# Kernel tuning notes

Measured on AMD Instinct MI355X. Metric: run time of the kernel, lower is better.

The kernel has to match this reference:

```python
import jax, jax.numpy as jnp
import numpy as np

B, T, LATENT, D, N_ENVS = 128, 64, 16, 512, 4
TOPK_RATIO = 0.1
TEMPERATURE = 1.0


def setup_inputs() -> dict:
    key = jax.random.key(0)
    k1, k2, k3, k4 = jax.random.split(key, 4)
    z_s = jax.random.normal(k1, (B, T, LATENT), dtype=jnp.float32)
    env_idx = jax.random.randint(k2, (B,), 0, N_ENVS, dtype=jnp.int64 if jax.config.jax_enable_x64 else jnp.int32)
    A_base = jax.random.normal(k3, (D, D), dtype=jnp.float32) * 0.1
    A_deltas = jax.random.normal(k4, (N_ENVS, D, D), dtype=jnp.float32) * 0.01  # stacked ParameterList
    return {"z_s": z_s, "env_idx": env_idx, "A_base": A_base, "A_deltas": A_deltas}


def reference(z_s, env_idx, A_base, A_deltas):
    b = z_s.shape[0]
    d = A_base.shape[0]
    # Per-env delta add: the torch loop sums delta_e * (env_idx==e) over envs,
    # which (one env per sample) equals a gather of A_deltas at env_idx.
    A_logits = A_base[None, :, :] + A_deltas[env_idx]          # [B, d, d]
    A_soft = jax.nn.sigmoid(A_logits / TEMPERATURE)            # [B, d, d]
    # Batched top-k sparsification (replaces the per-sample python loop).
    k = max(1, int(TOPK_RATIO * d * d))
    flat = A_logits.reshape(b, d * d)                          # [B, d*d]
    topk_vals, topk_idx = jax.lax.top_k(flat, k)               # [B, k]
    rows = jnp.arange(b)[:, None]                              # [B, 1]
    A_flat = jnp.zeros_like(flat).at[rows, topk_idx].set(jax.nn.sigmoid(topk_vals))
    A = A_flat.reshape(b, d, d)
    return A, A_logits, A_soft
```

## Files before the change

kernel.cpp:

```cpp
#include <hip/hip_runtime.h>
#include <stdint.h>

#define D_DIM   512
#define DD      262144
#define DD4     65536
#define B_DIM   128
#define N_ENVS  4
#define K_SEL   26214
#define BDD     33554432u
#define CAP2    65536
#define CAP3    4096

typedef float nfloat4 __attribute__((ext_vector_type(4)));

#define PK_OFF      64
#define CNT_OFF     128
#define HIST_OFF    192
#define HIST_BYTES  (N_ENVS * 256 * 4)
#define ZERO_BYTES  (HIST_OFF + HIST_BYTES - PK_OFF)
#define PAIRS_OFF   8192
#define PAIRS_BYTES ((size_t)N_ENVS * CAP2 * 8)
#define PLANES_OFF  (PAIRS_OFF + PAIRS_BYTES)
#define PLANES_BYTES ((size_t)N_ENVS * 3 * DD * 4)
#define WS_NEED     (PLANES_OFF + PLANES_BYTES)
#define SEL_NEED    (PAIRS_OFF + PAIRS_BYTES)

__device__ __forceinline__ uint32_t fkey(float f) {
    uint32_t u = __float_as_uint(f);
    return (u & 0x80000000u) ? ~u : (u | 0x80000000u);
}
__device__ __forceinline__ float sigmoidf_(float x) {
    return 1.0f / (1.0f + __expf(-x));
}

__global__ __launch_bounds__(256) void hist8_kernel(
    const float* __restrict__ base, const float* __restrict__ deltas,
    uint32_t* __restrict__ hist8)
{
    int e = blockIdx.y;
    const float4* b4 = (const float4*)base;
    const float4* d4 = (const float4*)(deltas + (size_t)e * DD);
    __shared__ uint32_t s_h[256];
    int tid = threadIdx.x;
    s_h[tid] = 0;
    __syncthreads();
    int g0 = blockIdx.x * 256 + tid;
    #pragma unroll
    for (int r = 0; r < 4; ++r) {
        int g = g0 + r * 16384;
        float4 bv = b4[g], dv = d4[g];
        atomicAdd(&s_h[fkey(bv.x + dv.x) >> 24], 1u);
        atomicAdd(&s_h[fkey(bv.y + dv.y) >> 24], 1u);
        atomicAdd(&s_h[fkey(bv.z + dv.z) >> 24], 1u);
        atomicAdd(&s_h[fkey(bv.w + dv.w) >> 24], 1u);
    }
    __syncthreads();
    if (s_h[tid]) atomicAdd(&hist8[e * 256 + tid], s_h[tid]);
}

__global__ __launch_bounds__(256) void gather8_kernel(
    const float* __restrict__ base, const float* __restrict__ deltas,
    const uint32_t* __restrict__ hist8, uint32_t* __restrict__ pk,
    uint32_t* __restrict__ cnt8, uint2* __restrict__ pairs8)
{
    int e = blockIdx.y;
    const float4* b4 = (const float4*)base;
    const float4* d4 = (const float4*)(deltas + (size_t)e * DD);
    uint2* pp = pairs8 + (size_t)e * CAP2;
    __shared__ uint32_t s_h[256];
    __shared__ uint32_t s_scan[256];
    __shared__ uint32_t s_P, s_base;
    int tid = threadIdx.x;

    s_h[tid] = hist8[e * 256 + tid];
    __syncthreads();
    if (tid == 0) {
        uint32_t cum = 0;
        for (int b = 255; b >= 0; --b) {
            uint32_t c = s_h[b];
            if (cum + c >= (uint32_t)K_SEL) {
                s_P = (uint32_t)b;
                if (blockIdx.x == 0) {
                    pk[2 * e + 0] = (uint32_t)b;
                    pk[2 * e + 1] = (uint32_t)K_SEL - cum;
                }
                break;
            }
            cum += c;
        }
    }
    __syncthreads();
    uint32_t P = s_P;

    int g0 = blockIdx.x * 256 + tid;
    uint32_t m = 0;
    #pragma unroll
    for (int r = 0; r < 4; ++r) {
        int g = g0 + r * 16384;
        float4 bv = b4[g], dv = d4[g];
        m += ((fkey(bv.x + dv.x) >> 24) == P);
        m += ((fkey(bv.y + dv.y) >> 24) == P);
        m += ((fkey(bv.z + dv.z) >> 24) == P);
        m += ((fkey(bv.w + dv.w) >> 24) == P);
    }
    s_scan[tid] = m;
    __syncthreads();
    #pragma unroll
    for (int off = 1; off < 256; off <<= 1) {
        uint32_t v = (tid >= off) ? s_scan[tid - off] : 0u;
        __syncthreads();
        s_scan[tid] += v;
        __syncthreads();
    }
    uint32_t excl = s_scan[tid] - m;
    if (tid == 255) s_base = atomicAdd(&cnt8[e], s_scan[255]);
    __syncthreads();
    uint32_t pos = s_base + excl;

    #pragma unroll
    for (int r = 0; r < 4; ++r) {
        int g = g0 + r * 16384;
        float4 bv = b4[g], dv = d4[g];
        float vs[4] = {bv.x + dv.x, bv.y + dv.y, bv.z + dv.z, bv.w + dv.w};
        #pragma unroll
        for (int j = 0; j < 4; ++j) {
            uint32_t key = fkey(vs[j]);
            if ((key >> 24) == P) {
                if (pos < CAP2) pp[pos] = make_uint2(key, (uint32_t)(g * 4 + j));
                ++pos;
            }
        }
    }
}

__global__ __launch_bounds__(1024) void select2_kernel(
    const uint32_t* __restrict__ pk, const uint32_t* __restrict__ cnt8,
    const uint2* __restrict__ pairs8, uint32_t* __restrict__ thrcut)
{
    int e = blockIdx.x;
    const uint2* pp = pairs8 + (size_t)e * CAP2;
    uint32_t M = cnt8[e]; if (M > CAP2) M = CAP2;
    uint32_t krem8 = pk[2 * e + 1];

    __shared__ uint32_t s_h16[256];
    __shared__ uint2    s_pairs[CAP3];
    __shared__ uint32_t s_b16, s_krem16, s_cnt;
    int tid = threadIdx.x;
    if (tid < 256) s_h16[tid] = 0;
    if (tid == 0) s_cnt = 0;
    __syncthreads();

    for (uint32_t j = tid; j < M; j += 1024)
        atomicAdd(&s_h16[(pp[j].x >> 16) & 255u], 1u);
    __syncthreads();
    if (tid == 0) {
        uint32_t cum = 0;
        for (int b = 255; b >= 0; --b) {
            uint32_t c = s_h16[b];
            if (cum + c >= krem8) { s_b16 = (uint32_t)b; s_krem16 = krem8 - cum; break; }
            cum += c;
        }
    }
    __syncthreads();
    uint32_t b16 = s_b16;
    for (uint32_t j = tid; j < M; j += 1024) {
        uint2 p = pp[j];
        if (((p.x >> 16) & 255u) == b16) {
            uint32_t pos = atomicAdd(&s_cnt, 1u);
            if (pos < CAP3) s_pairs[pos] = p;
        }
    }
    __syncthreads();
    uint32_t M2 = s_cnt; if (M2 > CAP3) M2 = CAP3;
    uint32_t target = s_krem16 - 1;
    for (uint32_t j = tid; j < M2; j += 1024) {
        uint2 me = s_pairs[j];
        uint32_t rank = 0;
        for (uint32_t l = 0; l < M2; ++l) {
            uint2 o = s_pairs[l];
            rank += (o.x > me.x) || (o.x == me.x && o.y < me.y);
        }
        if (rank == target) {
            thrcut[2 * e + 0] = me.x;
            thrcut[2 * e + 1] = me.y;
        }
    }
}

__global__ __launch_bounds__(256) void planes_kernel(
    const float* __restrict__ base, const float* __restrict__ deltas,
    const uint32_t* __restrict__ thrcut, float* __restrict__ planes)
{
    int e = blockIdx.y;
    int g = blockIdx.x * 256 + threadIdx.x;
    uint32_t T = thrcut[2 * e], C = thrcut[2 * e + 1];
    uint32_t i0 = (uint32_t)g * 4u;
    float4 bv = ((const float4*)base)[g];
    float4 dv = ((const float4*)(deltas + (size_t)e * DD))[g];
    nfloat4 lg = { bv.x + dv.x, bv.y + dv.y, bv.z + dv.z, bv.w + dv.w };
    nfloat4 sg = { sigmoidf_(lg.x), sigmoidf_(lg.y),
                   sigmoidf_(lg.z), sigmoidf_(lg.w) };
    uint32_t kx = fkey(lg.x), ky = fkey(lg.y), kz = fkey(lg.z), kw = fkey(lg.w);
    nfloat4 av;
    av.x = (kx > T || (kx == T && i0 + 0u <= C)) ? sg.x : 0.0f;
    av.y = (ky > T || (ky == T && i0 + 1u <= C)) ? sg.y : 0.0f;
    av.z = (kz > T || (kz == T && i0 + 2u <= C)) ? sg.z : 0.0f;
    av.w = (kw > T || (kw == T && i0 + 3u <= C)) ? sg.w : 0.0f;
    nfloat4* pl = (nfloat4*)(planes + (size_t)e * 3 * DD);
    pl[g]           = av;
    pl[g + DD4]     = lg;
    pl[g + 2 * DD4] = sg;
}

__global__ __launch_bounds__(256) void broadcast_kernel(
    const int* __restrict__ env_idx, const float* __restrict__ planes,
    float* __restrict__ out)
{
    int b = blockIdx.y;
    int e = env_idx[b];
    int g = blockIdx.x * 256 + threadIdx.x;
    const nfloat4* pl = (const nfloat4*)(planes + (size_t)e * 3 * DD);
    nfloat4 av = pl[g], lg = pl[g + DD4], sg = pl[g + 2 * DD4];
    nfloat4* o = (nfloat4*)out + (size_t)b * DD4 + g;
    __builtin_nontemporal_store(av, o);
    __builtin_nontemporal_store(lg, o + (BDD / 4));
    __builtin_nontemporal_store(sg, o + 2ull * (BDD / 4));
}

__global__ __launch_bounds__(256) void fused_write_kernel(
    const int* __restrict__ env_idx, const float* __restrict__ base,
    const float* __restrict__ deltas, const uint32_t* __restrict__ thrcut,
    float* __restrict__ out)
{
    int b = blockIdx.y;
    int e = env_idx[b];
    uint32_t T = thrcut[2 * e], C = thrcut[2 * e + 1];
    int g = blockIdx.x * 256 + threadIdx.x;
    uint32_t i0 = (uint32_t)g * 4u;
    float4 bv = ((const float4*)base)[g];
    float4 dv = ((const float4*)(deltas + (size_t)e * DD))[g];
    nfloat4 lg = { bv.x + dv.x, bv.y + dv.y, bv.z + dv.z, bv.w + dv.w };
    nfloat4 sg = { sigmoidf_(lg.x), sigmoidf_(lg.y),
                   sigmoidf_(lg.z), sigmoidf_(lg.w) };
    uint32_t kx = fkey(lg.x), ky = fkey(lg.y), kz = fkey(lg.z), kw = fkey(lg.w);
    nfloat4 av;
    av.x = (kx > T || (kx == T && i0 + 0u <= C)) ? sg.x : 0.0f;
    av.y = (ky > T || (ky == T && i0 + 1u <= C)) ? sg.y : 0.0f;
    av.z = (kz > T || (kz == T && i0 + 2u <= C)) ? sg.z : 0.0f;
    av.w = (kw > T || (kw == T && i0 + 3u <= C)) ? sg.w : 0.0f;
    size_t o = (size_t)b * DD4 + (size_t)g;
    nfloat4* o4 = (nfloat4*)out;
    __builtin_nontemporal_store(av, o4 + o);
    __builtin_nontemporal_store(lg, o4 + o + (BDD / 4));
    __builtin_nontemporal_store(sg, o4 + o + 2ull * (BDD / 4));
}

extern "C" void kernel_launch(void* const* d_in, const int* in_sizes, int n_in,
                              void* d_out, int out_size, void* d_ws, size_t ws_size,
                              hipStream_t stream) {
    const int*   env_idx  = (const int*)d_in[1];
    const float* A_base   = (const float*)d_in[2];
    const float* A_deltas = (const float*)d_in[3];
    float* out = (float*)d_out;

    uint32_t* thrcut = (uint32_t*)d_ws;

    bool plane_path = (ws_size >= WS_NEED);
    char* scratch;
    if (ws_size >= SEL_NEED) {
        scratch = (char*)d_ws;
    } else {
        size_t out_bytes = (size_t)out_size * sizeof(float);
        scratch = (char*)d_out + ((out_bytes - SEL_NEED) & ~(size_t)255);
        plane_path = false;
    }
    uint32_t* pk     = (uint32_t*)(scratch + PK_OFF);
    uint32_t* cnt8   = (uint32_t*)(scratch + CNT_OFF);
    uint32_t* hist8  = (uint32_t*)(scratch + HIST_OFF);
    uint2*    pairs8 = (uint2*)   (scratch + PAIRS_OFF);
    float*    planes = (float*)((char*)d_ws + PLANES_OFF);

    (void)hipMemsetAsync(scratch + PK_OFF, 0, ZERO_BYTES, stream);

    hist8_kernel  <<<dim3(64, N_ENVS), 256, 0, stream>>>(A_base, A_deltas, hist8);
    gather8_kernel<<<dim3(64, N_ENVS), 256, 0, stream>>>(A_base, A_deltas, hist8,
                                                         pk, cnt8, pairs8);
    select2_kernel<<<N_ENVS, 1024, 0, stream>>>(pk, cnt8, pairs8, thrcut);
    if (plane_path) {
        planes_kernel   <<<dim3(DD4 / 256, N_ENVS), 256, 0, stream>>>(
            A_base, A_deltas, thrcut, planes);
        broadcast_kernel<<<dim3(DD4 / 256, B_DIM),  256, 0, stream>>>(
            env_idx, planes, out);
    } else {
        fused_write_kernel<<<dim3(DD4 / 256, B_DIM), 256, 0, stream>>>(
            env_idx, A_base, A_deltas, thrcut, out);
    }
}
```

Baseline: 466.4 us.

## Drop memset and plane staging; use per-block histograms and register-cached keys

Replaces the global atomic histogram with per-block partial histograms that the gather kernel reduces, which removes the memset launch; cnt8 is now reset inside the histogram kernel. The gather kernel keeps the computed keys in registers instead of reloading base and deltas for its second pass. The precomputed planes plus broadcast path is removed, and the fused write kernel always recomputes logits and sigmoid per batch, with each thread handling two float4 groups. This trades the planes round-trip and one launch for redundant sigmoid work across the batch.

```diff
diff --git a/kernel.cpp b/kernel.cpp
--- a/kernel.cpp
+++ b/kernel.cpp
@@ -8,6 +8,7 @@
 #define N_ENVS  4
 #define K_SEL   26214
 #define BDD     33554432u
+#define NBLK    64
 #define CAP2    65536
 #define CAP3    4096
 
@@ -15,14 +16,10 @@
 
 #define PK_OFF      64
 #define CNT_OFF     128
-#define HIST_OFF    192
-#define HIST_BYTES  (N_ENVS * 256 * 4)
-#define ZERO_BYTES  (HIST_OFF + HIST_BYTES - PK_OFF)
-#define PAIRS_OFF   8192
+#define HISTP_OFF   4096
+#define HISTP_BYTES (NBLK * N_ENVS * 256 * 4)
+#define PAIRS_OFF   (512 * 1024)
 #define PAIRS_BYTES ((size_t)N_ENVS * CAP2 * 8)
-#define PLANES_OFF  (PAIRS_OFF + PAIRS_BYTES)
-#define PLANES_BYTES ((size_t)N_ENVS * 3 * DD * 4)
-#define WS_NEED     (PLANES_OFF + PLANES_BYTES)
 #define SEL_NEED    (PAIRS_OFF + PAIRS_BYTES)
 
 __device__ __forceinline__ uint32_t fkey(float f) {
@@ -35,7 +32,7 @@
 
 __global__ __launch_bounds__(256) void hist8_kernel(
     const float* __restrict__ base, const float* __restrict__ deltas,
-    uint32_t* __restrict__ hist8)
+    uint32_t* __restrict__ histp, uint32_t* __restrict__ cnt8)
 {
     int e = blockIdx.y;
     const float4* b4 = (const float4*)base;
@@ -43,6 +40,7 @@
     __shared__ uint32_t s_h[256];
     int tid = threadIdx.x;
     s_h[tid] = 0;
+    if (blockIdx.x == 0 && tid == 0) cnt8[e] = 0;
     __syncthreads();
     int g0 = blockIdx.x * 256 + tid;
     #pragma unroll
@@ -55,12 +53,12 @@
         atomicAdd(&s_h[fkey(bv.w + dv.w) >> 24], 1u);
     }
     __syncthreads();
-    if (s_h[tid]) atomicAdd(&hist8[e * 256 + tid], s_h[tid]);
+    histp[(blockIdx.x * N_ENVS + e) * 256 + tid] = s_h[tid];
 }
 
 __global__ __launch_bounds__(256) void gather8_kernel(
     const float* __restrict__ base, const float* __restrict__ deltas,
-    const uint32_t* __restrict__ hist8, uint32_t* __restrict__ pk,
+    const uint32_t* __restrict__ histp, uint32_t* __restrict__ pk,
     uint32_t* __restrict__ cnt8, uint2* __restrict__ pairs8)
 {
     int e = blockIdx.y;
@@ -72,7 +70,11 @@
     __shared__ uint32_t s_P, s_base;
     int tid = threadIdx.x;
 
-    s_h[tid] = hist8[e * 256 + tid];
+    uint32_t sum = 0;
+    #pragma unroll 8
+    for (int j = 0; j < NBLK; ++j)
+        sum += histp[(j * N_ENVS + e) * 256 + tid];
+    s_h[tid] = sum;
     __syncthreads();
     if (tid == 0) {
         uint32_t cum = 0;
@@ -93,15 +95,18 @@
     uint32_t P = s_P;
 
     int g0 = blockIdx.x * 256 + tid;
+    uint32_t keys[16];
     uint32_t m = 0;
     #pragma unroll
     for (int r = 0; r < 4; ++r) {
         int g = g0 + r * 16384;
         float4 bv = b4[g], dv = d4[g];
-        m += ((fkey(bv.x + dv.x) >> 24) == P);
-        m += ((fkey(bv.y + dv.y) >> 24) == P);
-        m += ((fkey(bv.z + dv.z) >> 24) == P);
-        m += ((fkey(bv.w + dv.w) >> 24) == P);
+        uint32_t k0 = fkey(bv.x + dv.x), k1 = fkey(bv.y + dv.y);
+        uint32_t k2 = fkey(bv.z + dv.z), k3 = fkey(bv.w + dv.w);
+        keys[r * 4 + 0] = k0; keys[r * 4 + 1] = k1;
+        keys[r * 4 + 2] = k2; keys[r * 4 + 3] = k3;
+        m += ((k0 >> 24) == P) + ((k1 >> 24) == P)
+           + ((k2 >> 24) == P) + ((k3 >> 24) == P);
     }
     s_scan[tid] = m;
     __syncthreads();
@@ -120,11 +125,9 @@
     #pragma unroll
     for (int r = 0; r < 4; ++r) {
         int g = g0 + r * 16384;
-        float4 bv = b4[g], dv = d4[g];
-        float vs[4] = {bv.x + dv.x, bv.y + dv.y, bv.z + dv.z, bv.w + dv.w};
         #pragma unroll
         for (int j = 0; j < 4; ++j) {
-            uint32_t key = fkey(vs[j]);
+            uint32_t key = keys[r * 4 + j];
             if ((key >> 24) == P) {
                 if (pos < CAP2) pp[pos] = make_uint2(key, (uint32_t)(g * 4 + j));
                 ++pos;
@@ -187,46 +190,6 @@
     }
 }
 
-__global__ __launch_bounds__(256) void planes_kernel(
-    const float* __restrict__ base, const float* __restrict__ deltas,
-    const uint32_t* __restrict__ thrcut, float* __restrict__ planes)
-{
-    int e = blockIdx.y;
-    int g = blockIdx.x * 256 + threadIdx.x;
-    uint32_t T = thrcut[2 * e], C = thrcut[2 * e + 1];
-    uint32_t i0 = (uint32_t)g * 4u;
-    float4 bv = ((const float4*)base)[g];
-    float4 dv = ((const float4*)(deltas + (size_t)e * DD))[g];
-    nfloat4 lg = { bv.x + dv.x, bv.y + dv.y, bv.z + dv.z, bv.w + dv.w };
-    nfloat4 sg = { sigmoidf_(lg.x), sigmoidf_(lg.y),
-                   sigmoidf_(lg.z), sigmoidf_(lg.w) };
-    uint32_t kx = fkey(lg.x), ky = fkey(lg.y), kz = fkey(lg.z), kw = fkey(lg.w);
-    nfloat4 av;
-    av.x = (kx > T || (kx == T && i0 + 0u <= C)) ? sg.x : 0.0f;
-    av.y = (ky > T || (ky == T && i0 + 1u <= C)) ? sg.y : 0.0f;
-    av.z = (kz > T || (kz == T && i0 + 2u <= C)) ? sg.z : 0.0f;
-    av.w = (kw > T || (kw == T && i0 + 3u <= C)) ? sg.w : 0.0f;
-    nfloat4* pl = (nfloat4*)(planes + (size_t)e * 3 * DD);
-    pl[g]           = av;
-    pl[g + DD4]     = lg;
-    pl[g + 2 * DD4] = sg;
-}
-
-__global__ __launch_bounds__(256) void broadcast_kernel(
-    const int* __restrict__ env_idx, const float* __restrict__ planes,
-    float* __restrict__ out)
-{
-    int b = blockIdx.y;
-    int e = env_idx[b];
-    int g = blockIdx.x * 256 + threadIdx.x;
-    const nfloat4* pl = (const nfloat4*)(planes + (size_t)e * 3 * DD);
-    nfloat4 av = pl[g], lg = pl[g + DD4], sg = pl[g + 2 * DD4];
-    nfloat4* o = (nfloat4*)out + (size_t)b * DD4 + g;
-    __builtin_nontemporal_store(av, o);
-    __builtin_nontemporal_store(lg, o + (BDD / 4));
-    __builtin_nontemporal_store(sg, o + 2ull * (BDD / 4));
-}
-
 __global__ __launch_bounds__(256) void fused_write_kernel(
     const int* __restrict__ env_idx, const float* __restrict__ base,
     const float* __restrict__ deltas, const uint32_t* __restrict__ thrcut,
@@ -235,24 +198,29 @@
     int b = blockIdx.y;
     int e = env_idx[b];
     uint32_t T = thrcut[2 * e], C = thrcut[2 * e + 1];
-    int g = blockIdx.x * 256 + threadIdx.x;
-    uint32_t i0 = (uint32_t)g * 4u;
-    float4 bv = ((const float4*)base)[g];
-    float4 dv = ((const float4*)(deltas + (size_t)e * DD))[g];
-    nfloat4 lg = { bv.x + dv.x, bv.y + dv.y, bv.z + dv.z, bv.w + dv.w };
-    nfloat4 sg = { sigmoidf_(lg.x), sigmoidf_(lg.y),
-                   sigmoidf_(lg.z), sigmoidf_(lg.w) };
-    uint32_t kx = fkey(lg.x), ky = fkey(lg.y), kz = fkey(lg.z), kw = fkey(lg.w);
-    nfloat4 av;
-    av.x = (kx > T || (kx == T && i0 + 0u <= C)) ? sg.x : 0.0f;
-    av.y = (ky > T || (ky == T && i0 + 1u <= C)) ? sg.y : 0.0f;
-    av.z = (kz > T || (kz == T && i0 + 2u <= C)) ? sg.z : 0.0f;
-    av.w = (kw > T || (kw == T && i0 + 3u <= C)) ? sg.w : 0.0f;
-    size_t o = (size_t)b * DD4 + (size_t)g;
-    nfloat4* o4 = (nfloat4*)out;
-    __builtin_nontemporal_store(av, o4 + o);
-    __builtin_nontemporal_store(lg, o4 + o + (BDD / 4));
-    __builtin_nontemporal_store(sg, o4 + o + 2ull * (BDD / 4));
+    const float4* b4 = (const float4*)base;
+    const float4* d4 = (const float4*)(deltas + (size_t)e * DD);
+    nfloat4* o4 = (nfloat4*)out + (size_t)b * DD4;
+    int g0 = blockIdx.x * 512 + threadIdx.x;
+    #pragma unroll
+    for (int r = 0; r < 2; ++r) {
+        int g = g0 + r * 256;
+        uint32_t i0 = (uint32_t)g * 4u;
+        float4 bv = b4[g];
+        float4 dv = d4[g];
+        nfloat4 lg = { bv.x + dv.x, bv.y + dv.y, bv.z + dv.z, bv.w + dv.w };
+        nfloat4 sg = { sigmoidf_(lg.x), sigmoidf_(lg.y),
+                       sigmoidf_(lg.z), sigmoidf_(lg.w) };
+        uint32_t kx = fkey(lg.x), ky = fkey(lg.y), kz = fkey(lg.z), kw = fkey(lg.w);
+        nfloat4 av;
+        av.x = (kx > T || (kx == T && i0 + 0u <= C)) ? sg.x : 0.0f;
+        av.y = (ky > T || (ky == T && i0 + 1u <= C)) ? sg.y : 0.0f;
+        av.z = (kz > T || (kz == T && i0 + 2u <= C)) ? sg.z : 0.0f;
+        av.w = (kw > T || (kw == T && i0 + 3u <= C)) ? sg.w : 0.0f;
+        __builtin_nontemporal_store(av, o4 + g);
+        __builtin_nontemporal_store(lg, o4 + g + (BDD / 4));
+        __builtin_nontemporal_store(sg, o4 + g + 2ull * (BDD / 4));
+    }
 }
 
 extern "C" void kernel_launch(void* const* d_in, const int* in_sizes, int n_in,
@@ -265,34 +233,23 @@
 
     uint32_t* thrcut = (uint32_t*)d_ws;
 
-    bool plane_path = (ws_size >= WS_NEED);
     char* scratch;
     if (ws_size >= SEL_NEED) {
         scratch = (char*)d_ws;
     } else {
         size_t out_bytes = (size_t)out_size * sizeof(float);
         scratch = (char*)d_out + ((out_bytes - SEL_NEED) & ~(size_t)255);
-        plane_path = false;
     }
     uint32_t* pk     = (uint32_t*)(scratch + PK_OFF);
     uint32_t* cnt8   = (uint32_t*)(scratch + CNT_OFF);
-    uint32_t* hist8  = (uint32_t*)(scratch + HIST_OFF);
+    uint32_t* histp  = (uint32_t*)(scratch + HISTP_OFF);
     uint2*    pairs8 = (uint2*)   (scratch + PAIRS_OFF);
-    float*    planes = (float*)((char*)d_ws + PLANES_OFF);
-
-    (void)hipMemsetAsync(scratch + PK_OFF, 0, ZERO_BYTES, stream);
-
-    hist8_kernel  <<<dim3(64, N_ENVS), 256, 0, stream>>>(A_base, A_deltas, hist8);
-    gather8_kernel<<<dim3(64, N_ENVS), 256, 0, stream>>>(A_base, A_deltas, hist8,
-                                                         pk, cnt8, pairs8);
+
+    hist8_kernel  <<<dim3(NBLK, N_ENVS), 256, 0, stream>>>(A_base, A_deltas,
+                                                           histp, cnt8);
+    gather8_kernel<<<dim3(NBLK, N_ENVS), 256, 0, stream>>>(A_base, A_deltas, histp,
+                                                           pk, cnt8, pairs8);
     select2_kernel<<<N_ENVS, 1024, 0, stream>>>(pk, cnt8, pairs8, thrcut);
-    if (plane_path) {
-        planes_kernel   <<<dim3(DD4 / 256, N_ENVS), 256, 0, stream>>>(
-            A_base, A_deltas, thrcut, planes);
-        broadcast_kernel<<<dim3(DD4 / 256, B_DIM),  256, 0, stream>>>(
-            env_idx, planes, out);
-    } else {
-        fused_write_kernel<<<dim3(DD4 / 256, B_DIM), 256, 0, stream>>>(
-            env_idx, A_base, A_deltas, thrcut, out);
-    }
-}
+    fused_write_kernel<<<dim3(DD4 / 512, B_DIM), 256, 0, stream>>>(
+        env_idx, A_base, A_deltas, thrcut, out);
+}
```

New measurement: 461.6 us. About the same (-1.0%).
